# Kernel tuning notes

Hardware: AMD Instinct MI355X
Metric: run time of the kernel (lower is better)

The kernel has to match this reference:

```python
import jax, jax.numpy as jnp
import numpy as np

N_NODES = 50000
N_EDGES = 800000
IN_DIM = 64
HID = 256
EDGE_DIM = 6
NEG_SLOPE = 0.2


def setup_inputs() -> dict:
    key = jax.random.key(0)
    ks = jax.random.split(key, 16)
    glorot = lambda k, shp: jax.random.normal(k, shp, jnp.float32) * jnp.sqrt(2.0 / (shp[0] + shp[-1]))
    x = jax.random.normal(ks[0], (N_NODES, IN_DIM), jnp.float32)
    edge_index = jax.random.randint(ks[1], (2, N_EDGES), 0, N_NODES, dtype=jnp.int32)
    edge_attr = jax.random.normal(ks[2], (N_EDGES, EDGE_DIM), jnp.float32)
    return {
        "x": x,
        "edge_index": edge_index,
        "edge_attr": edge_attr,
        # layer 1 (heads=1)
        "W1": glorot(ks[3], (IN_DIM, HID)),
        "att_src1": glorot(ks[4], (HID,)),
        "att_dst1": glorot(ks[5], (HID,)),
        "We1": glorot(ks[6], (EDGE_DIM, HID)),
        "att_e1": glorot(ks[7], (HID,)),
        "b1": jnp.zeros((HID,), jnp.float32),
        # layer 2
        "W2": glorot(ks[8], (HID, HID)),
        "att_src2": glorot(ks[9], (HID,)),
        "att_dst2": glorot(ks[10], (HID,)),
        "We2": glorot(ks[11], (EDGE_DIM, HID)),
        "att_e2": glorot(ks[12], (HID,)),
        "b2": jnp.zeros((HID,), jnp.float32),
    }


def gat_conv(x, src, dst, edge_attr, W, att_src, att_dst, We, att_e, b):
    # PyG GATConv, heads=1, add_self_loops=False, edge features in attention only
    h = x @ W                              # [N, C]
    a_src = h @ att_src                    # [N]
    a_dst = h @ att_dst                    # [N]
    a_edge = (edge_attr @ We) @ att_e      # [E]
    alpha = a_src[src] + a_dst[dst] + a_edge            # [E]
    alpha = jax.nn.leaky_relu(alpha, NEG_SLOPE)
    # softmax over edges sharing the same destination node
    amax = jax.ops.segment_max(alpha, dst, num_segments=N_NODES)
    amax = jnp.where(jnp.isneginf(amax), 0.0, amax)
    ex = jnp.exp(alpha - amax[dst])
    denom = jax.ops.segment_sum(ex, dst, num_segments=N_NODES)
    alpha = ex / (denom[dst] + 1e-16)
    msg = h[src] * alpha[:, None]          # [E, C]
    out = jax.ops.segment_sum(msg, dst, num_segments=N_NODES)  # [N, C]
    return out + b


def reference(x, edge_index, edge_attr, W1, att_src1, att_dst1, We1, att_e1, b1,
              W2, att_src2, att_dst2, We2, att_e2, b2):
    src, dst = edge_index[0], edge_index[1]
    h = jax.nn.relu(gat_conv(x, src, dst, edge_attr, W1, att_src1, att_dst1, We1, att_e1, b1))
    # dropout(p=0.2) is identity in eval mode
    out = gat_conv(h, src, dst, edge_attr, W2, att_src2, att_dst2, We2, att_e2, b2)
    return out  # out_proj is Identity (out_dim=None)
```

## Files before the change

### kernel.cpp

```cpp
#include <hip/hip_runtime.h>
#include <hip/hip_bf16.h>

#define N_NODES_C 50000
#define N_EDGES_C 800000
#define IN_DIM_C 64
#define HID_C 256
#define EDGE_DIM_C 6
#define NEG_SLOPE_C 0.2f

typedef short short8 __attribute__((ext_vector_type(8)));
typedef float f32x4 __attribute__((ext_vector_type(4)));

static __device__ __forceinline__ float b2f(unsigned short u) {
    union { unsigned int i; float f; } x;
    x.i = ((unsigned int)u) << 16;
    return x.f;
}
static __device__ __forceinline__ unsigned short f2b(float f) {
    union { __hip_bfloat16 h; unsigned short u; } x;
    x.h = __float2bfloat16(f);
    return x.u;
}

__global__ void k_prep(const float* __restrict__ W1, const float* __restrict__ W2,
                       unsigned short* __restrict__ W1t, unsigned short* __restrict__ W2t,
                       const float* __restrict__ We1, const float* __restrict__ atte1,
                       const float* __restrict__ We2, const float* __restrict__ atte2,
                       float* __restrict__ v) {
    int tid = threadIdx.x;
    int i = blockIdx.x * blockDim.x + tid;
    if (i < IN_DIM_C * HID_C) {
        int k = i >> 8, n = i & 255;
        W1t[n * IN_DIM_C + k] = f2b(W1[i]);
    }
    if (i < HID_C * HID_C) {
        int k = i >> 8, n = i & 255;
        W2t[n * HID_C + k] = f2b(W2[i]);
    }
    if (blockIdx.x == 255) {
        __shared__ float red[256];
        for (int layer = 0; layer < 2; ++layer) {
            const float* We = layer ? We2 : We1;
            const float* ae = layer ? atte2 : atte1;
            for (int k = 0; k < EDGE_DIM_C; ++k) {
                red[tid] = We[k * HID_C + tid] * ae[tid];
                __syncthreads();
                for (int s = 128; s > 0; s >>= 1) {
                    if (tid < s) red[tid] += red[tid + s];
                    __syncthreads();
                }
                if (tid == 0) v[layer * 8 + k] = red[0];
                __syncthreads();
            }
        }
    }
}

__global__ void k_pre(const int* __restrict__ dst, const float* __restrict__ eattr,
                      const float* __restrict__ v, int* __restrict__ deg,
                      float* __restrict__ ae1, float* __restrict__ ae2) {
    int e = blockIdx.x * blockDim.x + threadIdx.x;
    if (e >= N_EDGES_C) return;
    atomicAdd(&deg[dst[e]], 1);
    float a1 = 0.f, a2 = 0.f;
#pragma unroll
    for (int k = 0; k < EDGE_DIM_C; ++k) {
        float ea = eattr[e * EDGE_DIM_C + k];
        a1 += ea * v[k];
        a2 += ea * v[8 + k];
    }
    ae1[e] = a1;
    ae2[e] = a2;
}

__global__ void k_scan1(const int* __restrict__ deg, int* __restrict__ offs,
                        int* __restrict__ bsum) {
    __shared__ int tmp[256];
    int b = blockIdx.x, tid = threadIdx.x;
    int i = b * 256 + tid;
    int v = (i < N_NODES_C) ? deg[i] : 0;
    tmp[tid] = v;
    __syncthreads();
    for (int d = 1; d < 256; d <<= 1) {
        int t = (tid >= d) ? tmp[tid - d] : 0;
        __syncthreads();
        tmp[tid] += t;
        __syncthreads();
    }
    if (i < N_NODES_C) offs[i] = tmp[tid] - v;
    if (tid == 255) bsum[b] = tmp[255];
}
__global__ void k_scan2(const int* __restrict__ bsum, int* __restrict__ boff, int nb) {
    __shared__ int tmp[256];
    int tid = threadIdx.x;
    int v = (tid < nb) ? bsum[tid] : 0;
    tmp[tid] = v;
    __syncthreads();
    for (int d = 1; d < 256; d <<= 1) {
        int t = (tid >= d) ? tmp[tid - d] : 0;
        __syncthreads();
        tmp[tid] += t;
        __syncthreads();
    }
    if (tid < nb) boff[tid] = tmp[tid] - v;
}
__global__ void k_scan3(int* __restrict__ offs, const int* __restrict__ boff,
                        int* __restrict__ cur) {
    int b = blockIdx.x, tid = threadIdx.x;
    int i = b * 256 + tid;
    if (i < N_NODES_C) {
        int o = offs[i] + boff[b];
        offs[i] = o;
        cur[i] = o;
    }
    if (i == 0) offs[N_NODES_C] = N_EDGES_C;
}

__global__ void k_perm(const int* __restrict__ dst, int* __restrict__ cur,
                       int* __restrict__ perm) {
    int e = blockIdx.x * blockDim.x + threadIdx.x;
    if (e >= N_EDGES_C) return;
    int pos = atomicAdd(&cur[dst[e]], 1);
    perm[pos] = e;
}

__global__ void k_gather(const int* __restrict__ perm, const int* __restrict__ src,
                         const float* __restrict__ ae1, const float* __restrict__ ae2,
                         int* __restrict__ ssrc, float* __restrict__ sae1,
                         float* __restrict__ sae2) {
    int p = blockIdx.x * blockDim.x + threadIdx.x;
    if (p >= N_EDGES_C) return;
    int e = perm[p];
    ssrc[p] = src[e];
    sae1[p] = ae1[e];
    sae2[p] = ae2[e];
}

template <int KT, bool SRCF32>
__global__ __launch_bounds__(256) void k_gemm_mfma(const void* __restrict__ Xv,
                                                   const unsigned short* __restrict__ Wt,
                                                   unsigned short* __restrict__ H,
                                                   const float* __restrict__ att_s,
                                                   const float* __restrict__ att_d,
                                                   float* __restrict__ asrc,
                                                   float* __restrict__ adst) {
    __shared__ unsigned short As[64 * 64];
    __shared__ unsigned short Bs[256 * 64];
    __shared__ float ds[4][64];
    __shared__ float dd[4][64];
    int tid = threadIdx.x;
    int w = tid >> 6, l = tid & 63;
    int lr = l & 15, lg = l >> 4;
    long mbase = (long)blockIdx.x * 64;

    float asv[4], adv[4];
#pragma unroll
    for (int ni = 0; ni < 4; ++ni) {
        int col = w * 64 + ni * 16 + lr;
        asv[ni] = att_s[col];
        adv[ni] = att_d[col];
    }

    f32x4 acc[4][4];
#pragma unroll
    for (int mi = 0; mi < 4; ++mi)
#pragma unroll
        for (int ni = 0; ni < 4; ++ni) acc[mi][ni] = (f32x4){0.f, 0.f, 0.f, 0.f};

    for (int k0 = 0; k0 < KT; k0 += 64) {
#pragma unroll
        for (int p = 0; p < 2; ++p) {
            int r = p * 32 + (tid >> 3);
            int c8 = tid & 7;
            long row = mbase + r;
            short8 val = {0, 0, 0, 0, 0, 0, 0, 0};
            if (row < N_NODES_C) {
                if (SRCF32) {
                    const float* Xf = (const float*)Xv;
                    const f32x4* p4 = (const f32x4*)&Xf[row * KT + k0 + c8 * 8];
                    f32x4 a0 = p4[0], a1 = p4[1];
#pragma unroll
                    for (int q = 0; q < 4; ++q) val[q] = (short)f2b(a0[q]);
#pragma unroll
                    for (int q = 0; q < 4; ++q) val[4 + q] = (short)f2b(a1[q]);
                } else {
                    const unsigned short* Xb = (const unsigned short*)Xv;
                    val = *(const short8*)&Xb[row * KT + k0 + c8 * 8];
                }
            }
            *(short8*)&As[r * 64 + ((c8 ^ (r & 7)) * 8)] = val;
        }
        {
            int n = tid;
#pragma unroll
            for (int c8 = 0; c8 < 8; ++c8) {
                *(short8*)&Bs[n * 64 + ((c8 ^ (n & 7)) * 8)] =
                    *(const short8*)&Wt[(long)n * KT + k0 + c8 * 8];
            }
        }
        __syncthreads();
#pragma unroll
        for (int kk = 0; kk < 2; ++kk) {
            int cblk = kk * 4 + lg;
            short8 a[4], b[4];
#pragma unroll
            for (int mi = 0; mi < 4; ++mi) {
                int R = mi * 16 + lr;
                a[mi] = *(const short8*)&As[R * 64 + ((cblk ^ (R & 7)) * 8)];
            }
#pragma unroll
            for (int ni = 0; ni < 4; ++ni) {
                int Nr = w * 64 + ni * 16 + lr;
                b[ni] = *(const short8*)&Bs[Nr * 64 + ((cblk ^ (Nr & 7)) * 8)];
            }
#pragma unroll
            for (int mi = 0; mi < 4; ++mi)
#pragma unroll
                for (int ni = 0; ni < 4; ++ni)
                    acc[mi][ni] = __builtin_amdgcn_mfma_f32_16x16x32_bf16(a[mi], b[ni],
                                                                          acc[mi][ni], 0, 0, 0);
        }
        __syncthreads();
    }

#pragma unroll
    for (int mi = 0; mi < 4; ++mi) {
#pragma unroll
        for (int r = 0; r < 4; ++r) {
            int rowl = mi * 16 + lg * 4 + r;
            long row = mbase + rowl;
            float ps = 0.f, pd = 0.f;
#pragma unroll
            for (int ni = 0; ni < 4; ++ni) {
                float h = acc[mi][ni][r];
                ps += h * asv[ni];
                pd += h * adv[ni];
            }
#pragma unroll
            for (int o = 1; o < 16; o <<= 1) {
                ps += __shfl_xor(ps, o, 16);
                pd += __shfl_xor(pd, o, 16);
            }
            if (lr == 0) {
                ds[w][rowl] = ps;
                dd[w][rowl] = pd;
            }
            if (row < N_NODES_C) {
#pragma unroll
                for (int ni = 0; ni < 4; ++ni) {
                    H[row * HID_C + w * 64 + ni * 16 + lr] = f2b(acc[mi][ni][r]);
                }
            }
        }
    }
    __syncthreads();
    if (tid < 64) {
        long row = mbase + tid;
        if (row < N_NODES_C) {
            asrc[row] = ds[0][tid] + ds[1][tid] + ds[2][tid] + ds[3][tid];
            adst[row] = dd[0][tid] + dd[1][tid] + dd[2][tid] + dd[3][tid];
        }
    }
}

__global__ __launch_bounds__(256) void k_aggr2(const int* __restrict__ offs,
                                               const int* __restrict__ ssrc,
                                               const float* __restrict__ sae,
                                               const float* __restrict__ asrc,
                                               const float* __restrict__ adst,
                                               const unsigned short* __restrict__ H,
                                               const float* __restrict__ bias,
                                               void* __restrict__ outp, int mode) {
    int tid = threadIdx.x;
    int hw = tid >> 5;
    int l = tid & 31;
    int node = blockIdx.x * 8 + hw;
    int off0 = offs[node];
    int deg = offs[node + 1] - off0;
    float adi = adst[node];

    int sidx0 = 0, sidx1 = 0;
    float w0 = 0.f, w1 = 0.f;
    if (l < deg) {
        sidx0 = ssrc[off0 + l];
        float a = asrc[sidx0] + adi + sae[off0 + l];
        a = (a > 0.f) ? a : NEG_SLOPE_C * a;
        w0 = __expf(a);
    }
    if (32 + l < deg) {
        sidx1 = ssrc[off0 + 32 + l];
        float a = asrc[sidx1] + adi + sae[off0 + 32 + l];
        a = (a > 0.f) ? a : NEG_SLOPE_C * a;
        w1 = __expf(a);
    }
    float s = w0 + w1;
    for (int j = 64 + l; j < deg; j += 32) {
        int si = ssrc[off0 + j];
        float a = asrc[si] + adi + sae[off0 + j];
        a = (a > 0.f) ? a : NEG_SLOPE_C * a;
        s += __expf(a);
    }
#pragma unroll
    for (int o = 16; o > 0; o >>= 1) s += __shfl_xor(s, o, 32);
    float inv = 1.0f / (s + 1e-16f);

    int c8 = l * 8;
    float acc[8];
#pragma unroll
    for (int q = 0; q < 8; ++q) acc[q] = 0.f;

    auto fetch = [&](int j, int& si, float& wv) {
        if (j < 32) {
            si = __shfl(sidx0, j, 32);
            wv = __shfl(w0, j, 32);
        } else if (j < 64) {
            si = __shfl(sidx1, j - 32, 32);
            wv = __shfl(w1, j - 32, 32);
        } else {
            si = ssrc[off0 + j];
            float a = asrc[si] + adi + sae[off0 + j];
            a = (a > 0.f) ? a : NEG_SLOPE_C * a;
            wv = __expf(a);
        }
    };

    int j = 0;
    for (; j + 7 < deg; j += 8) {
        int ii[8];
        float uu[8];
#pragma unroll
        for (int q = 0; q < 8; ++q) fetch(j + q, ii[q], uu[q]);
        short8 h[8];
#pragma unroll
        for (int q = 0; q < 8; ++q) h[q] = *(const short8*)&H[(long)ii[q] * HID_C + c8];
#pragma unroll
        for (int t = 0; t < 8; ++t)
#pragma unroll
            for (int q = 0; q < 8; ++q) acc[q] += uu[t] * b2f((unsigned short)h[t][q]);
    }
    for (; j + 3 < deg; j += 4) {
        int ii[4];
        float uu[4];
#pragma unroll
        for (int q = 0; q < 4; ++q) fetch(j + q, ii[q], uu[q]);
        short8 h[4];
#pragma unroll
        for (int q = 0; q < 4; ++q) h[q] = *(const short8*)&H[(long)ii[q] * HID_C + c8];
#pragma unroll
        for (int t = 0; t < 4; ++t)
#pragma unroll
            for (int q = 0; q < 8; ++q) acc[q] += uu[t] * b2f((unsigned short)h[t][q]);
    }
    for (; j < deg; ++j) {
        int i0;
        float u0;
        fetch(j, i0, u0);
        short8 h0 = *(const short8*)&H[(long)i0 * HID_C + c8];
#pragma unroll
        for (int q = 0; q < 8; ++q) acc[q] += u0 * b2f((unsigned short)h0[q]);
    }

    const f32x4* b4 = (const f32x4*)&bias[c8];
    f32x4 bv0 = b4[0], bv1 = b4[1];
    if (mode == 1) {
        unsigned short* o16 = (unsigned short*)outp;
        short8 r;
#pragma unroll
        for (int q = 0; q < 4; ++q)
            r[q] = (short)f2b(fmaxf(acc[q] * inv + bv0[q], 0.f));
#pragma unroll
        for (int q = 0; q < 4; ++q)
            r[4 + q] = (short)f2b(fmaxf(acc[4 + q] * inv + bv1[q], 0.f));
        *(short8*)&o16[(long)node * HID_C + c8] = r;
    } else {
        float* o32 = (float*)outp;
        f32x4 r0, r1;
#pragma unroll
        for (int q = 0; q < 4; ++q) r0[q] = acc[q] * inv + bv0[q];
#pragma unroll
        for (int q = 0; q < 4; ++q) r1[q] = acc[4 + q] * inv + bv1[q];
        *(f32x4*)&o32[(long)node * HID_C + c8] = r0;
        *(f32x4*)&o32[(long)node * HID_C + c8 + 4] = r1;
    }
}

extern "C" void kernel_launch(void* const* d_in, const int* in_sizes, int n_in,
                              void* d_out, int out_size, void* d_ws, size_t ws_size,
                              hipStream_t stream) {
    const float* x     = (const float*)d_in[0];
    const int*   ei    = (const int*)d_in[1];
    const float* eattr = (const float*)d_in[2];
    const float* W1    = (const float*)d_in[3];
    const float* atts1 = (const float*)d_in[4];
    const float* attd1 = (const float*)d_in[5];
    const float* We1   = (const float*)d_in[6];
    const float* atte1 = (const float*)d_in[7];
    const float* b1    = (const float*)d_in[8];
    const float* W2    = (const float*)d_in[9];
    const float* atts2 = (const float*)d_in[10];
    const float* attd2 = (const float*)d_in[11];
    const float* We2   = (const float*)d_in[12];
    const float* atte2 = (const float*)d_in[13];
    const float* b2    = (const float*)d_in[14];
    float* out = (float*)d_out;

    char* ws = (char*)d_ws;
    size_t off = 0;
    auto alloc = [&](size_t bytes) -> void* {
        void* p = ws + off;
        off = (off + bytes + 255) & ~(size_t)255;
        return p;
    };
    int*   deg  = (int*)alloc((size_t)N_NODES_C * 4);
    int*   offs = (int*)alloc(((size_t)N_NODES_C + 1) * 4);
    int*   cur  = (int*)alloc((size_t)N_NODES_C * 4);
    int*   perm = (int*)alloc((size_t)N_EDGES_C * 4);
    int*   ssrc = (int*)alloc((size_t)N_EDGES_C * 4);
    float* ae1  = (float*)alloc((size_t)N_EDGES_C * 4);
    float* ae2  = (float*)alloc((size_t)N_EDGES_C * 4);
    float* sae1 = (float*)alloc((size_t)N_EDGES_C * 4);
    float* sae2 = (float*)alloc((size_t)N_EDGES_C * 4);
    float* asrc = (float*)alloc((size_t)N_NODES_C * 4);
    float* adst = (float*)alloc((size_t)N_NODES_C * 4);
    float* v    = (float*)alloc(64);
    int*   bsum = (int*)alloc(256 * 4);
    int*   boff = (int*)alloc(257 * 4);
    unsigned short* W1t = (unsigned short*)alloc((size_t)HID_C * IN_DIM_C * 2);
    unsigned short* W2t = (unsigned short*)alloc((size_t)HID_C * HID_C * 2);
    unsigned short* h1  = (unsigned short*)alloc((size_t)N_NODES_C * HID_C * 2);
    unsigned short* g1  = (unsigned short*)alloc((size_t)N_NODES_C * HID_C * 2);

    const int* src = ei;
    const int* dst = ei + N_EDGES_C;
    int nb = (N_NODES_C + 255) / 256;

    hipMemsetAsync(deg, 0, (size_t)N_NODES_C * 4, stream);

    k_prep<<<256, 256, 0, stream>>>(W1, W2, W1t, W2t, We1, atte1, We2, atte2, v);
    k_pre<<<(N_EDGES_C + 255) / 256, 256, 0, stream>>>(dst, eattr, v, deg, ae1, ae2);
    k_scan1<<<nb, 256, 0, stream>>>(deg, offs, bsum);
    k_scan2<<<1, 256, 0, stream>>>(bsum, boff, nb);
    k_scan3<<<nb, 256, 0, stream>>>(offs, boff, cur);
    k_perm<<<(N_EDGES_C + 255) / 256, 256, 0, stream>>>(dst, cur, perm);
    k_gather<<<(N_EDGES_C + 255) / 256, 256, 0, stream>>>(perm, src, ae1, ae2,
                                                          ssrc, sae1, sae2);

    int gemm_grid = (N_NODES_C + 63) / 64;
    k_gemm_mfma<IN_DIM_C, true><<<gemm_grid, 256, 0, stream>>>(x, W1t, h1, atts1, attd1,
                                                               asrc, adst);
    k_aggr2<<<N_NODES_C / 8, 256, 0, stream>>>(offs, ssrc, sae1, asrc, adst, h1, b1, g1, 1);
    k_gemm_mfma<HID_C, false><<<gemm_grid, 256, 0, stream>>>(g1, W2t, h1, atts2, attd2,
                                                             asrc, adst);
    k_aggr2<<<N_NODES_C / 8, 256, 0, stream>>>(offs, ssrc, sae2, asrc, adst, h1, b2, out, 0);
}
```

Before: 306.1 us.

## Split aggregation into normalization pass and column-sliced gather with packed edge records

```diff
diff --git a/kernel.cpp b/kernel.cpp
--- a/kernel.cpp
+++ b/kernel.cpp
@@ -263,124 +263,91 @@
     }
 }
 
-__global__ __launch_bounds__(256) void k_aggr2(const int* __restrict__ offs,
-                                               const int* __restrict__ ssrc,
-                                               const float* __restrict__ sae,
-                                               const float* __restrict__ asrc,
-                                               const float* __restrict__ adst,
-                                               const unsigned short* __restrict__ H,
-                                               const float* __restrict__ bias,
-                                               void* __restrict__ outp, int mode) {
+__global__ __launch_bounds__(256) void k_norm(const int* __restrict__ offs,
+                                              const int* __restrict__ ssrc,
+                                              const float* __restrict__ sae,
+                                              const float* __restrict__ asrc,
+                                              const float* __restrict__ adst,
+                                              float* __restrict__ wts,
+                                              unsigned int* __restrict__ enc) {
     int tid = threadIdx.x;
-    int hw = tid >> 5;
-    int l = tid & 31;
+    int hw = tid >> 5, l = tid & 31;
     int node = blockIdx.x * 8 + hw;
     int off0 = offs[node];
     int deg = offs[node + 1] - off0;
     float adi = adst[node];
-
-    int sidx0 = 0, sidx1 = 0;
-    float w0 = 0.f, w1 = 0.f;
-    if (l < deg) {
-        sidx0 = ssrc[off0 + l];
-        float a = asrc[sidx0] + adi + sae[off0 + l];
-        a = (a > 0.f) ? a : NEG_SLOPE_C * a;
-        w0 = __expf(a);
-    }
-    if (32 + l < deg) {
-        sidx1 = ssrc[off0 + 32 + l];
-        float a = asrc[sidx1] + adi + sae[off0 + 32 + l];
-        a = (a > 0.f) ? a : NEG_SLOPE_C * a;
-        w1 = __expf(a);
-    }
-    float s = w0 + w1;
-    for (int j = 64 + l; j < deg; j += 32) {
+    float s = 0.f;
+    for (int j = l; j < deg; j += 32) {
         int si = ssrc[off0 + j];
         float a = asrc[si] + adi + sae[off0 + j];
         a = (a > 0.f) ? a : NEG_SLOPE_C * a;
-        s += __expf(a);
+        float w = __expf(a);
+        wts[off0 + j] = w;
+        s += w;
     }
 #pragma unroll
     for (int o = 16; o > 0; o >>= 1) s += __shfl_xor(s, o, 32);
     float inv = 1.0f / (s + 1e-16f);
-
-    int c8 = l * 8;
-    float acc[8];
-#pragma unroll
-    for (int q = 0; q < 8; ++q) acc[q] = 0.f;
-
-    auto fetch = [&](int j, int& si, float& wv) {
-        if (j < 32) {
-            si = __shfl(sidx0, j, 32);
-            wv = __shfl(w0, j, 32);
-        } else if (j < 64) {
-            si = __shfl(sidx1, j - 32, 32);
-            wv = __shfl(w1, j - 32, 32);
-        } else {
-            si = ssrc[off0 + j];
-            float a = asrc[si] + adi + sae[off0 + j];
-            a = (a > 0.f) ? a : NEG_SLOPE_C * a;
-            wv = __expf(a);
-        }
-    };
-
+    for (int j = l; j < deg; j += 32) {
+        unsigned int sv = ((unsigned int)ssrc[off0 + j]) << 16;
+        enc[off0 + j] = sv | (unsigned int)f2b(wts[off0 + j] * inv);
+    }
+}
+
+__global__ __launch_bounds__(256) void k_aggrslice(const int* __restrict__ offs,
+                                                   const unsigned int* __restrict__ enc,
+                                                   const unsigned short* __restrict__ H,
+                                                   const float* __restrict__ bias,
+                                                   void* __restrict__ outp, int mode) {
+    int tid = threadIdx.x;
+    int slice = blockIdx.x & 7;
+    int grp = blockIdx.x >> 3;
+    int g = tid >> 4;
+    int l = tid & 15;
+    int node = grp * 16 + g;
+    int off0 = offs[node];
+    int deg = offs[node + 1] - off0;
+    int ce = slice * 32 + l * 2;
+    const unsigned int* ep = enc + off0;
+
+    float a0 = 0.f, a1 = 0.f;
     int j = 0;
-    for (; j + 7 < deg; j += 8) {
-        int ii[8];
-        float uu[8];
-#pragma unroll
-        for (int q = 0; q < 8; ++q) fetch(j + q, ii[q], uu[q]);
-        short8 h[8];
-#pragma unroll
-        for (int q = 0; q < 8; ++q) h[q] = *(const short8*)&H[(long)ii[q] * HID_C + c8];
-#pragma unroll
-        for (int t = 0; t < 8; ++t)
-#pragma unroll
-            for (int q = 0; q < 8; ++q) acc[q] += uu[t] * b2f((unsigned short)h[t][q]);
-    }
     for (; j + 3 < deg; j += 4) {
-        int ii[4];
-        float uu[4];
-#pragma unroll
-        for (int q = 0; q < 4; ++q) fetch(j + q, ii[q], uu[q]);
-        short8 h[4];
-#pragma unroll
-        for (int q = 0; q < 4; ++q) h[q] = *(const short8*)&H[(long)ii[q] * HID_C + c8];
-#pragma unroll
-        for (int t = 0; t < 4; ++t)
-#pragma unroll
-            for (int q = 0; q < 8; ++q) acc[q] += uu[t] * b2f((unsigned short)h[t][q]);
+        unsigned int e0 = __builtin_nontemporal_load(ep + j);
+        unsigned int e1 = __builtin_nontemporal_load(ep + j + 1);
+        unsigned int e2 = __builtin_nontemporal_load(ep + j + 2);
+        unsigned int e3 = __builtin_nontemporal_load(ep + j + 3);
+        ushort2 h0 = *(const ushort2*)&H[(e0 >> 16) * HID_C + ce];
+        ushort2 h1 = *(const ushort2*)&H[(e1 >> 16) * HID_C + ce];
+        ushort2 h2 = *(const ushort2*)&H[(e2 >> 16) * HID_C + ce];
+        ushort2 h3 = *(const ushort2*)&H[(e3 >> 16) * HID_C + ce];
+        float w0 = b2f((unsigned short)(e0 & 0xffffu));
+        float w1 = b2f((unsigned short)(e1 & 0xffffu));
+        float w2 = b2f((unsigned short)(e2 & 0xffffu));
+        float w3 = b2f((unsigned short)(e3 & 0xffffu));
+        a0 += w0 * b2f(h0.x) + w1 * b2f(h1.x) + w2 * b2f(h2.x) + w3 * b2f(h3.x);
+        a1 += w0 * b2f(h0.y) + w1 * b2f(h1.y) + w2 * b2f(h2.y) + w3 * b2f(h3.y);
     }
     for (; j < deg; ++j) {
-        int i0;
-        float u0;
-        fetch(j, i0, u0);
-        short8 h0 = *(const short8*)&H[(long)i0 * HID_C + c8];
-#pragma unroll
-        for (int q = 0; q < 8; ++q) acc[q] += u0 * b2f((unsigned short)h0[q]);
-    }
-
-    const f32x4* b4 = (const f32x4*)&bias[c8];
-    f32x4 bv0 = b4[0], bv1 = b4[1];
+        unsigned int e0 = __builtin_nontemporal_load(ep + j);
+        ushort2 h0 = *(const ushort2*)&H[(e0 >> 16) * HID_C + ce];
+        float w0 = b2f((unsigned short)(e0 & 0xffffu));
+        a0 += w0 * b2f(h0.x);
+        a1 += w0 * b2f(h0.y);
+    }
+
+    float r0 = a0 + bias[ce];
+    float r1 = a1 + bias[ce + 1];
     if (mode == 1) {
-        unsigned short* o16 = (unsigned short*)outp;
-        short8 r;
-#pragma unroll
-        for (int q = 0; q < 4; ++q)
-            r[q] = (short)f2b(fmaxf(acc[q] * inv + bv0[q], 0.f));
-#pragma unroll
-        for (int q = 0; q < 4; ++q)
-            r[4 + q] = (short)f2b(fmaxf(acc[4 + q] * inv + bv1[q], 0.f));
-        *(short8*)&o16[(long)node * HID_C + c8] = r;
+        ushort2 r;
+        r.x = f2b(fmaxf(r0, 0.f));
+        r.y = f2b(fmaxf(r1, 0.f));
+        *(ushort2*)&((unsigned short*)outp)[(long)node * HID_C + ce] = r;
     } else {
-        float* o32 = (float*)outp;
-        f32x4 r0, r1;
-#pragma unroll
-        for (int q = 0; q < 4; ++q) r0[q] = acc[q] * inv + bv0[q];
-#pragma unroll
-        for (int q = 0; q < 4; ++q) r1[q] = acc[4 + q] * inv + bv1[q];
-        *(f32x4*)&o32[(long)node * HID_C + c8] = r0;
-        *(f32x4*)&o32[(long)node * HID_C + c8 + 4] = r1;
+        float2 r;
+        r.x = r0;
+        r.y = r1;
+        *(float2*)&((float*)outp)[(long)node * HID_C + ce] = r;
     }
 }
 
@@ -430,6 +397,9 @@
     unsigned short* h1  = (unsigned short*)alloc((size_t)N_NODES_C * HID_C * 2);
     unsigned short* g1  = (unsigned short*)alloc((size_t)N_NODES_C * HID_C * 2);
 
+    float*        wts = ae1;
+    unsigned int* enc = (unsigned int*)ae2;
+
     const int* src = ei;
     const int* dst = ei + N_EDGES_C;
     int nb = (N_NODES_C + 255) / 256;
@@ -446,10 +416,13 @@
                                                           ssrc, sae1, sae2);
 
     int gemm_grid = (N_NODES_C + 63) / 64;
+    int aggr_grid = (N_NODES_C / 16) * 8;
     k_gemm_mfma<IN_DIM_C, true><<<gemm_grid, 256, 0, stream>>>(x, W1t, h1, atts1, attd1,
                                                                asrc, adst);
-    k_aggr2<<<N_NODES_C / 8, 256, 0, stream>>>(offs, ssrc, sae1, asrc, adst, h1, b1, g1, 1);
+    k_norm<<<N_NODES_C / 8, 256, 0, stream>>>(offs, ssrc, sae1, asrc, adst, wts, enc);
+    k_aggrslice<<<aggr_grid, 256, 0, stream>>>(offs, enc, h1, b1, g1, 1);
     k_gemm_mfma<HID_C, false><<<gemm_grid, 256, 0, stream>>>(g1, W2t, h1, atts2, attd2,
                                                              asrc, adst);
-    k_aggr2<<<N_NODES_C / 8, 256, 0, stream>>>(offs, ssrc, sae2, asrc, adst, h1, b2, out, 0);
-}
+    k_norm<<<N_NODES_C / 8, 256, 0, stream>>>(offs, ssrc, sae2, asrc, adst, wts, enc);
+    k_aggrslice<<<aggr_grid, 256, 0, stream>>>(offs, enc, h1, b2, out, 0);
+}
```

Result: slower. 504.5 us (+64.8%).

## Fuse layer-1 aggregation into layer-2 GEMM and merge edge prep with GEMM1

Applied to the files above, without the earlier changes.

```diff
diff --git a/kernel.cpp b/kernel.cpp
--- a/kernel.cpp
+++ b/kernel.cpp
@@ -22,13 +22,102 @@
     return x.u;
 }
 
+static __device__ __forceinline__ float aggr_node(int off0, int deg, float adi,
+                                                  const int* __restrict__ ssrc,
+                                                  const float* __restrict__ sae,
+                                                  const float* __restrict__ asrc,
+                                                  const unsigned short* __restrict__ H,
+                                                  int l, float* acc) {
+    int sidx0 = 0, sidx1 = 0;
+    float w0 = 0.f, w1 = 0.f;
+    if (l < deg) {
+        sidx0 = ssrc[off0 + l];
+        float a = asrc[sidx0] + adi + sae[off0 + l];
+        a = (a > 0.f) ? a : NEG_SLOPE_C * a;
+        w0 = __expf(a);
+    }
+    if (32 + l < deg) {
+        sidx1 = ssrc[off0 + 32 + l];
+        float a = asrc[sidx1] + adi + sae[off0 + 32 + l];
+        a = (a > 0.f) ? a : NEG_SLOPE_C * a;
+        w1 = __expf(a);
+    }
+    float s = w0 + w1;
+    for (int j = 64 + l; j < deg; j += 32) {
+        int si = ssrc[off0 + j];
+        float a = asrc[si] + adi + sae[off0 + j];
+        a = (a > 0.f) ? a : NEG_SLOPE_C * a;
+        s += __expf(a);
+    }
+#pragma unroll
+    for (int o = 16; o > 0; o >>= 1) s += __shfl_xor(s, o, 32);
+    float inv = 1.0f / (s + 1e-16f);
+
+    int c8 = l * 8;
+#pragma unroll
+    for (int q = 0; q < 8; ++q) acc[q] = 0.f;
+
+    auto fetch = [&](int j, int& si, float& wv) {
+        if (j < 32) {
+            si = __shfl(sidx0, j, 32);
+            wv = __shfl(w0, j, 32);
+        } else if (j < 64) {
+            si = __shfl(sidx1, j - 32, 32);
+            wv = __shfl(w1, j - 32, 32);
+        } else {
+            si = ssrc[off0 + j];
+            float a = asrc[si] + adi + sae[off0 + j];
+            a = (a > 0.f) ? a : NEG_SLOPE_C * a;
+            wv = __expf(a);
+        }
+    };
+
+    int j = 0;
+    for (; j + 7 < deg; j += 8) {
+        int ii[8];
+        float uu[8];
+#pragma unroll
+        for (int q = 0; q < 8; ++q) fetch(j + q, ii[q], uu[q]);
+        short8 h[8];
+#pragma unroll
+        for (int q = 0; q < 8; ++q) h[q] = *(const short8*)&H[(long)ii[q] * HID_C + c8];
+#pragma unroll
+        for (int t = 0; t < 8; ++t)
+#pragma unroll
+            for (int q = 0; q < 8; ++q) acc[q] += uu[t] * b2f((unsigned short)h[t][q]);
+    }
+    for (; j + 3 < deg; j += 4) {
+        int ii[4];
+        float uu[4];
+#pragma unroll
+        for (int q = 0; q < 4; ++q) fetch(j + q, ii[q], uu[q]);
+        short8 h[4];
+#pragma unroll
+        for (int q = 0; q < 4; ++q) h[q] = *(const short8*)&H[(long)ii[q] * HID_C + c8];
+#pragma unroll
+        for (int t = 0; t < 4; ++t)
+#pragma unroll
+            for (int q = 0; q < 8; ++q) acc[q] += uu[t] * b2f((unsigned short)h[t][q]);
+    }
+    for (; j < deg; ++j) {
+        int i0;
+        float u0;
+        fetch(j, i0, u0);
+        short8 h0 = *(const short8*)&H[(long)i0 * HID_C + c8];
+#pragma unroll
+        for (int q = 0; q < 8; ++q) acc[q] += u0 * b2f((unsigned short)h0[q]);
+    }
+    return inv;
+}
+
 __global__ void k_prep(const float* __restrict__ W1, const float* __restrict__ W2,
                        unsigned short* __restrict__ W1t, unsigned short* __restrict__ W2t,
                        const float* __restrict__ We1, const float* __restrict__ atte1,
                        const float* __restrict__ We2, const float* __restrict__ atte2,
-                       float* __restrict__ v) {
+                       float* __restrict__ v, int* __restrict__ deg) {
     int tid = threadIdx.x;
     int i = blockIdx.x * blockDim.x + tid;
+    if (i < N_NODES_C) deg[i] = 0;
     if (i < IN_DIM_C * HID_C) {
         int k = i >> 8, n = i & 255;
         W1t[n * IN_DIM_C + k] = f2b(W1[i]);
@@ -56,21 +145,143 @@
     }
 }
 
-__global__ void k_pre(const int* __restrict__ dst, const float* __restrict__ eattr,
-                      const float* __restrict__ v, int* __restrict__ deg,
-                      float* __restrict__ ae1, float* __restrict__ ae2) {
-    int e = blockIdx.x * blockDim.x + threadIdx.x;
-    if (e >= N_EDGES_C) return;
-    atomicAdd(&deg[dst[e]], 1);
-    float a1 = 0.f, a2 = 0.f;
-#pragma unroll
-    for (int k = 0; k < EDGE_DIM_C; ++k) {
-        float ea = eattr[e * EDGE_DIM_C + k];
-        a1 += ea * v[k];
-        a2 += ea * v[8 + k];
-    }
-    ae1[e] = a1;
-    ae2[e] = a2;
+#define GEMM1_BLOCKS 782
+
+__global__ __launch_bounds__(256) void k_pre_gemm1(
+    const float* __restrict__ X, const unsigned short* __restrict__ Wt,
+    unsigned short* __restrict__ H, const float* __restrict__ att_s,
+    const float* __restrict__ att_d, float* __restrict__ asrc,
+    float* __restrict__ adst,
+    const int* __restrict__ dst, const float* __restrict__ eattr,
+    const float* __restrict__ v, int* __restrict__ deg,
+    float* __restrict__ ae1, float* __restrict__ ae2) {
+    __shared__ unsigned short As[64 * 64];
+    __shared__ unsigned short Bs[256 * 64];
+    __shared__ float ds[4][64];
+    __shared__ float dd[4][64];
+    int tid = threadIdx.x;
+
+    if (blockIdx.x >= GEMM1_BLOCKS) {
+        int e = (blockIdx.x - GEMM1_BLOCKS) * 256 + tid;
+        if (e < N_EDGES_C) {
+            atomicAdd(&deg[dst[e]], 1);
+            float a1 = 0.f, a2 = 0.f;
+#pragma unroll
+            for (int k = 0; k < EDGE_DIM_C; ++k) {
+                float ea = eattr[e * EDGE_DIM_C + k];
+                a1 += ea * v[k];
+                a2 += ea * v[8 + k];
+            }
+            ae1[e] = a1;
+            ae2[e] = a2;
+        }
+        return;
+    }
+
+    int w = tid >> 6, l = tid & 63;
+    int lr = l & 15, lg = l >> 4;
+    long mbase = (long)blockIdx.x * 64;
+
+    float asv[4], adv[4];
+#pragma unroll
+    for (int ni = 0; ni < 4; ++ni) {
+        int col = w * 64 + ni * 16 + lr;
+        asv[ni] = att_s[col];
+        adv[ni] = att_d[col];
+    }
+
+    f32x4 acc[4][4];
+#pragma unroll
+    for (int mi = 0; mi < 4; ++mi)
+#pragma unroll
+        for (int ni = 0; ni < 4; ++ni) acc[mi][ni] = (f32x4){0.f, 0.f, 0.f, 0.f};
+
+    {
+#pragma unroll
+        for (int p = 0; p < 2; ++p) {
+            int r = p * 32 + (tid >> 3);
+            int c8 = tid & 7;
+            long row = mbase + r;
+            short8 val = {0, 0, 0, 0, 0, 0, 0, 0};
+            if (row < N_NODES_C) {
+                const f32x4* p4 = (const f32x4*)&X[row * IN_DIM_C + c8 * 8];
+                f32x4 a0 = p4[0], a1 = p4[1];
+#pragma unroll
+                for (int q = 0; q < 4; ++q) val[q] = (short)f2b(a0[q]);
+#pragma unroll
+                for (int q = 0; q < 4; ++q) val[4 + q] = (short)f2b(a1[q]);
+            }
+            *(short8*)&As[r * 64 + ((c8 ^ (r & 7)) * 8)] = val;
+        }
+        int n = tid;
+#pragma unroll
+        for (int c8 = 0; c8 < 8; ++c8) {
+            *(short8*)&Bs[n * 64 + ((c8 ^ (n & 7)) * 8)] =
+                *(const short8*)&Wt[(long)n * IN_DIM_C + c8 * 8];
+        }
+        __syncthreads();
+#pragma unroll
+        for (int kk = 0; kk < 2; ++kk) {
+            int cblk = kk * 4 + lg;
+            short8 a[4], b[4];
+#pragma unroll
+            for (int mi = 0; mi < 4; ++mi) {
+                int R = mi * 16 + lr;
+                a[mi] = *(const short8*)&As[R * 64 + ((cblk ^ (R & 7)) * 8)];
+            }
+#pragma unroll
+            for (int ni = 0; ni < 4; ++ni) {
+                int Nr = w * 64 + ni * 16 + lr;
+                b[ni] = *(const short8*)&Bs[Nr * 64 + ((cblk ^ (Nr & 7)) * 8)];
+            }
+#pragma unroll
+            for (int mi = 0; mi < 4; ++mi)
+#pragma unroll
+                for (int ni = 0; ni < 4; ++ni)
+                    acc[mi][ni] = __builtin_amdgcn_mfma_f32_16x16x32_bf16(a[mi], b[ni],
+                                                                          acc[mi][ni], 0, 0, 0);
+        }
+        __syncthreads();
+    }
+
+#pragma unroll
+    for (int mi = 0; mi < 4; ++mi) {
+#pragma unroll
+        for (int r = 0; r < 4; ++r) {
+            int rowl = mi * 16 + lg * 4 + r;
+            long row = mbase + rowl;
+            float ps = 0.f, pd = 0.f;
+#pragma unroll
+            for (int ni = 0; ni < 4; ++ni) {
+                float h = acc[mi][ni][r];
+                ps += h * asv[ni];
+                pd += h * adv[ni];
+            }
+#pragma unroll
+            for (int o = 1; o < 16; o <<= 1) {
+                ps += __shfl_xor(ps, o, 16);
+                pd += __shfl_xor(pd, o, 16);
+            }
+            if (lr == 0) {
+                ds[w][rowl] = ps;
+                dd[w][rowl] = pd;
+            }
+            if (row < N_NODES_C) {
+#pragma unroll
+                for (int ni = 0; ni < 4; ++ni) {
+                    H[row * HID_C + w * 64 + ni * 16 + lr] = f2b(acc[mi][ni][r]);
+                }
+            }
+        }
+    }
+    __syncthreads();
+    if (tid < 64) {
+        long row = mbase + tid;
+        if (row < N_NODES_C) {
+            asrc[row] = ds[0][tid] + ds[1][tid] + ds[2][tid] + ds[3][tid];
+            adst[row] = dd[0][tid] + dd[1][tid] + dd[2][tid] + dd[3][tid];
+        }
+    }
 }
 
 __global__ void k_scan1(const int* __restrict__ deg, int* __restrict__ offs,
@@ -136,22 +347,48 @@
     sae2[p] = ae2[e];
 }
 
-template <int KT, bool SRCF32>
-__global__ __launch_bounds__(256) void k_gemm_mfma(const void* __restrict__ Xv,
-                                                   const unsigned short* __restrict__ Wt,
-                                                   unsigned short* __restrict__ H,
-                                                   const float* __restrict__ att_s,
-                                                   const float* __restrict__ att_d,
-                                                   float* __restrict__ asrc,
-                                                   float* __restrict__ adst) {
-    __shared__ unsigned short As[64 * 64];
+__global__ __launch_bounds__(256) void k_aggr_gemm(
+    const int* __restrict__ offs, const int* __restrict__ ssrc,
+    const float* __restrict__ sae, const float* __restrict__ asrc,
+    const float* __restrict__ adst, const unsigned short* __restrict__ H,
+    const float* __restrict__ bias, const unsigned short* __restrict__ Wt,
+    unsigned short* __restrict__ H2, const float* __restrict__ att_s,
+    const float* __restrict__ att_d, float* __restrict__ asrc2,
+    float* __restrict__ adst2) {
+    __shared__ unsigned short As[64 * 256];
     __shared__ unsigned short Bs[256 * 64];
     __shared__ float ds[4][64];
     __shared__ float dd[4][64];
     int tid = threadIdx.x;
-    int w = tid >> 6, l = tid & 63;
-    int lr = l & 15, lg = l >> 4;
     long mbase = (long)blockIdx.x * 64;
+
+    int hw = tid >> 5, l = tid & 31;
+    int c8 = l * 8;
+    for (int p = 0; p < 8; ++p) {
+        int rowl = p * 8 + hw;
+        long node = mbase + rowl;
+        short8 rowv = {0, 0, 0, 0, 0, 0, 0, 0};
+        if (node < N_NODES_C) {
+            int off0 = offs[node];
+            int deg = offs[node + 1] - off0;
+            float adi = adst[node];
+            float acc[8];
+            float inv = aggr_node(off0, deg, adi, ssrc, sae, asrc, H, l, acc);
+            const f32x4* b4 = (const f32x4*)&bias[c8];
+            f32x4 bv0 = b4[0], bv1 = b4[1];
+#pragma unroll
+            for (int q = 0; q < 4; ++q)
+                rowv[q] = (short)f2b(fmaxf(acc[q] * inv + bv0[q], 0.f));
+#pragma unroll
+            for (int q = 0; q < 4; ++q)
+                rowv[4 + q] = (short)f2b(fmaxf(acc[4 + q] * inv + bv1[q], 0.f));
+        }
+        *(short8*)&As[rowl * 256 + (l >> 3) * 64 + (((l & 7) ^ (rowl & 7)) * 8)] = rowv;
+    }
+    __syncthreads();
+
+    int w = tid >> 6, l64 = tid & 63;
+    int lr = l64 & 15, lg = l64 >> 4;
 
     float asv[4], adv[4];
 #pragma unroll
@@ -167,36 +404,12 @@
 #pragma unroll
         for (int ni = 0; ni < 4; ++ni) acc[mi][ni] = (f32x4){0.f, 0.f, 0.f, 0.f};
 
-    for (int k0 = 0; k0 < KT; k0 += 64) {
-#pragma unroll
-        for (int p = 0; p < 2; ++p) {
-            int r = p * 32 + (tid >> 3);
-            int c8 = tid & 7;
-            long row = mbase + r;
-            short8 val = {0, 0, 0, 0, 0, 0, 0, 0};
-            if (row < N_NODES_C) {
-                if (SRCF32) {
-                    const float* Xf = (const float*)Xv;
-                    const f32x4* p4 = (const f32x4*)&Xf[row * KT + k0 + c8 * 8];
-                    f32x4 a0 = p4[0], a1 = p4[1];
-#pragma unroll
-                    for (int q = 0; q < 4; ++q) val[q] = (short)f2b(a0[q]);
-#pragma unroll
-                    for (int q = 0; q < 4; ++q) val[4 + q] = (short)f2b(a1[q]);
-                } else {
-                    const unsigned short* Xb = (const unsigned short*)Xv;
-                    val = *(const short8*)&Xb[row * KT + k0 + c8 * 8];
-                }
-            }
-            *(short8*)&As[r * 64 + ((c8 ^ (r & 7)) * 8)] = val;
-        }
-        {
-            int n = tid;
-#pragma unroll
-            for (int c8 = 0; c8 < 8; ++c8) {
-                *(short8*)&Bs[n * 64 + ((c8 ^ (n & 7)) * 8)] =
-                    *(const short8*)&Wt[(long)n * KT + k0 + c8 * 8];
-            }
+    for (int k0 = 0; k0 < HID_C; k0 += 64) {
+        int n = tid;
+#pragma unroll
+        for (int cb = 0; cb < 8; ++cb) {
+            *(short8*)&Bs[n * 64 + ((cb ^ (n & 7)) * 8)] =
+                *(const short8*)&Wt[(long)n * HID_C + k0 + cb * 8];
         }
         __syncthreads();
 #pragma unroll
@@ -206,7 +419,7 @@
 #pragma unroll
             for (int mi = 0; mi < 4; ++mi) {
                 int R = mi * 16 + lr;
-                a[mi] = *(const short8*)&As[R * 64 + ((cblk ^ (R & 7)) * 8)];
+                a[mi] = *(const short8*)&As[R * 256 + k0 + ((cblk ^ (R & 7)) * 8)];
             }
 #pragma unroll
             for (int ni = 0; ni < 4; ++ni) {
@@ -248,7 +461,7 @@
             if (row < N_NODES_C) {
 #pragma unroll
                 for (int ni = 0; ni < 4; ++ni) {
-                    H[row * HID_C + w * 64 + ni * 16 + lr] = f2b(acc[mi][ni][r]);
+                    H2[row * HID_C + w * 64 + ni * 16 + lr] = f2b(acc[mi][ni][r]);
                 }
             }
         }
@@ -257,8 +470,8 @@
     if (tid < 64) {
         long row = mbase + tid;
         if (row < N_NODES_C) {
-            asrc[row] = ds[0][tid] + ds[1][tid] + ds[2][tid] + ds[3][tid];
-            adst[row] = dd[0][tid] + dd[1][tid] + dd[2][tid] + dd[3][tid];
+            asrc2[row] = ds[0][tid] + ds[1][tid] + ds[2][tid] + ds[3][tid];
+            adst2[row] = dd[0][tid] + dd[1][tid] + dd[2][tid] + dd[3][tid];
         }
     }
 }
@@ -270,7 +483,7 @@
                                                const float* __restrict__ adst,
                                                const unsigned short* __restrict__ H,
                                                const float* __restrict__ bias,
-                                               void* __restrict__ outp, int mode) {
+                                               float* __restrict__ out) {
     int tid = threadIdx.x;
     int hw = tid >> 5;
     int l = tid & 31;
@@ -278,110 +491,18 @@
     int off0 = offs[node];
     int deg = offs[node + 1] - off0;
     float adi = adst[node];
-
-    int sidx0 = 0, sidx1 = 0;
-    float w0 = 0.f, w1 = 0.f;
-    if (l < deg) {
-        sidx0 = ssrc[off0 + l];
-        float a = asrc[sidx0] + adi + sae[off0 + l];
-        a = (a > 0.f) ? a : NEG_SLOPE_C * a;
-        w0 = __expf(a);
-    }
-    if (32 + l < deg) {
-        sidx1 = ssrc[off0 + 32 + l];
-        float a = asrc[sidx1] + adi + sae[off0 + 32 + l];
-        a = (a > 0.f) ? a : NEG_SLOPE_C * a;
-        w1 = __expf(a);
-    }
-    float s = w0 + w1;
-    for (int j = 64 + l; j < deg; j += 32) {
-        int si = ssrc[off0 + j];
-        float a = asrc[si] + adi + sae[off0 + j];
-        a = (a > 0.f) ? a : NEG_SLOPE_C * a;
-        s += __expf(a);
-    }
-#pragma unroll
-    for (int o = 16; o > 0; o >>= 1) s += __shfl_xor(s, o, 32);
-    float inv = 1.0f / (s + 1e-16f);
-
+    float acc[8];
+    float inv = aggr_node(off0, deg, adi, ssrc, sae, asrc, H, l, acc);
     int c8 = l * 8;
-    float acc[8];
-#pragma unroll
-    for (int q = 0; q < 8; ++q) acc[q] = 0.f;
-
-    auto fetch = [&](int j, int& si, float& wv) {
-        if (j < 32) {
-            si = __shfl(sidx0, j, 32);
-            wv = __shfl(w0, j, 32);
-        } else if (j < 64) {
-            si = __shfl(sidx1, j - 32, 32);
-            wv = __shfl(w1, j - 32, 32);
-        } else {
-            si = ssrc[off0 + j];
-            float a = asrc[si] + adi + sae[off0 + j];
-            a = (a > 0.f) ? a : NEG_SLOPE_C * a;
-            wv = __expf(a);
-        }
-    };
-
-    int j = 0;
-    for (; j + 7 < deg; j += 8) {
-        int ii[8];
-        float uu[8];
-#pragma unroll
-        for (int q = 0; q < 8; ++q) fetch(j + q, ii[q], uu[q]);
-        short8 h[8];
-#pragma unroll
-        for (int q = 0; q < 8; ++q) h[q] = *(const short8*)&H[(long)ii[q] * HID_C + c8];
-#pragma unroll
-        for (int t = 0; t < 8; ++t)
-#pragma unroll
-            for (int q = 0; q < 8; ++q) acc[q] += uu[t] * b2f((unsigned short)h[t][q]);
-    }
-    for (; j + 3 < deg; j += 4) {
-        int ii[4];
-        float uu[4];
-#pragma unroll
-        for (int q = 0; q < 4; ++q) fetch(j + q, ii[q], uu[q]);
-        short8 h[4];
-#pragma unroll
-        for (int q = 0; q < 4; ++q) h[q] = *(const short8*)&H[(long)ii[q] * HID_C + c8];
-#pragma unroll
-        for (int t = 0; t < 4; ++t)
-#pragma unroll
-            for (int q = 0; q < 8; ++q) acc[q] += uu[t] * b2f((unsigned short)h[t][q]);
-    }
-    for (; j < deg; ++j) {
-        int i0;
-        float u0;
-        fetch(j, i0, u0);
-        short8 h0 = *(const short8*)&H[(long)i0 * HID_C + c8];
-#pragma unroll
-        for (int q = 0; q < 8; ++q) acc[q] += u0 * b2f((unsigned short)h0[q]);
-    }
-
     const f32x4* b4 = (const f32x4*)&bias[c8];
     f32x4 bv0 = b4[0], bv1 = b4[1];
-    if (mode == 1) {
-        unsigned short* o16 = (unsigned short*)outp;
-        short8 r;
-#pragma unroll
-        for (int q = 0; q < 4; ++q)
-            r[q] = (short)f2b(fmaxf(acc[q] * inv + bv0[q], 0.f));
-#pragma unroll
-        for (int q = 0; q < 4; ++q)
-            r[4 + q] = (short)f2b(fmaxf(acc[4 + q] * inv + bv1[q], 0.f));
-        *(short8*)&o16[(long)node * HID_C + c8] = r;
-    } else {
-        float* o32 = (float*)outp;
-        f32x4 r0, r1;
-#pragma unroll
-        for (int q = 0; q < 4; ++q) r0[q] = acc[q] * inv + bv0[q];
-#pragma unroll
-        for (int q = 0; q < 4; ++q) r1[q] = acc[4 + q] * inv + bv1[q];
-        *(f32x4*)&o32[(long)node * HID_C + c8] = r0;
-        *(f32x4*)&o32[(long)node * HID_C + c8 + 4] = r1;
-    }
+    f32x4 r0, r1;
+#pragma unroll
+    for (int q = 0; q < 4; ++q) r0[q] = acc[q] * inv + bv0[q];
+#pragma unroll
+    for (int q = 0; q < 4; ++q) r1[q] = acc[4 + q] * inv + bv1[q];
+    *(f32x4*)&out[(long)node * HID_C + c8] = r0;
+    *(f32x4*)&out[(long)node * HID_C + c8 + 4] = r1;
 }
 
 extern "C" void kernel_launch(void* const* d_in, const int* in_sizes, int n_in,
@@ -411,45 +532,43 @@
         off = (off + bytes + 255) & ~(size_t)255;
         return p;
     };
-    int*   deg  = (int*)alloc((size_t)N_NODES_C * 4);
-    int*   offs = (int*)alloc(((size_t)N_NODES_C + 1) * 4);
-    int*   cur  = (int*)alloc((size_t)N_NODES_C * 4);
-    int*   perm = (int*)alloc((size_t)N_EDGES_C * 4);
-    int*   ssrc = (int*)alloc((size_t)N_EDGES_C * 4);
-    float* ae1  = (float*)alloc((size_t)N_EDGES_C * 4);
-    float* ae2  = (float*)alloc((size_t)N_EDGES_C * 4);
-    float* sae1 = (float*)alloc((size_t)N_EDGES_C * 4);
-    float* sae2 = (float*)alloc((size_t)N_EDGES_C * 4);
-    float* asrc = (float*)alloc((size_t)N_NODES_C * 4);
-    float* adst = (float*)alloc((size_t)N_NODES_C * 4);
-    float* v    = (float*)alloc(64);
-    int*   bsum = (int*)alloc(256 * 4);
-    int*   boff = (int*)alloc(257 * 4);
+    int*   deg   = (int*)alloc((size_t)N_NODES_C * 4);
+    int*   offs  = (int*)alloc(((size_t)N_NODES_C + 1) * 4);
+    int*   cur   = (int*)alloc((size_t)N_NODES_C * 4);
+    int*   perm  = (int*)alloc((size_t)N_EDGES_C * 4);
+    int*   ssrc  = (int*)alloc((size_t)N_EDGES_C * 4);
+    float* ae1   = (float*)alloc((size_t)N_EDGES_C * 4);
+    float* ae2   = (float*)alloc((size_t)N_EDGES_C * 4);
+    float* sae1  = (float*)alloc((size_t)N_EDGES_C * 4);
+    float* sae2  = (float*)alloc((size_t)N_EDGES_C * 4);
+    float* asrc  = (float*)alloc((size_t)N_NODES_C * 4);
+    float* adst  = (float*)alloc((size_t)N_NODES_C * 4);
+    float* asrc2 = (float*)alloc((size_t)N_NODES_C * 4);
+    float* adst2 = (float*)alloc((size_t)N_NODES_C * 4);
+    float* v     = (float*)alloc(64);
+    int*   bsum  = (int*)alloc(256 * 4);
+    int*   boff  = (int*)alloc(257 * 4);
     unsigned short* W1t = (unsigned short*)alloc((size_t)HID_C * IN_DIM_C * 2);
     unsigned short* W2t = (unsigned short*)alloc((size_t)HID_C * HID_C * 2);
     unsigned short* h1  = (unsigned short*)alloc((size_t)N_NODES_C * HID_C * 2);
-    unsigned short* g1  = (unsigned short*)alloc((size_t)N_NODES_C * HID_C * 2);
+    unsigned short* h2  = (unsigned short*)alloc((size_t)N_NODES_C * HID_C * 2);
 
     const int* src = ei;
     const int* dst = ei + N_EDGES_C;
     int nb = (N_NODES_C + 255) / 256;
-
-    hipMemsetAsync(deg, 0, (size_t)N_NODES_C * 4, stream);
-
-    k_prep<<<256, 256, 0, stream>>>(W1, W2, W1t, W2t, We1, atte1, We2, atte2, v);
-    k_pre<<<(N_EDGES_C + 255) / 256, 256, 0, stream>>>(dst, eattr, v, deg, ae1, ae2);
+    int pre_blocks = (N_EDGES_C + 255) / 256;
+    int gemm_grid = (N_NODES_C + 63) / 64;
+
+    k_prep<<<256, 256, 0, stream>>>(W1, W2, W1t, W2t, We1, atte1, We2, atte2, v, deg);
+    k_pre_gemm1<<<GEMM1_BLOCKS + pre_blocks, 256, 0, stream>>>(
+        x, W1t, h1, atts1, attd1, asrc, adst, dst, eattr, v, deg, ae1, ae2);
     k_scan1<<<nb, 256, 0, stream>>>(deg, offs, bsum);
     k_scan2<<<1, 256, 0, stream>>>(bsum, boff, nb);
     k_scan3<<<nb, 256, 0, stream>>>(offs, boff, cur);
-    k_perm<<<(N_EDGES_C + 255) / 256, 256, 0, stream>>>(dst, cur, perm);
-    k_gather<<<(N_EDGES_C + 255) / 256, 256, 0, stream>>>(perm, src, ae1, ae2,
-                                                          ssrc, sae1, sae2);
-
-    int gemm_grid = (N_NODES_C + 63) / 64;
-    k_gemm_mfma<IN_DIM_C, true><<<gemm_grid, 256, 0, stream>>>(x, W1t, h1, atts1, attd1,
-                                                               asrc, adst);
-    k_aggr2<<<N_NODES_C / 8, 256, 0, stream>>>(offs, ssrc, sae1, asrc, adst, h1, b1, g1, 1);
-    k_gemm_mfma<HID_C, false><<<gemm_grid, 256, 0, stream>>>(g1, W2t, h1, atts2, attd2,
-                                                             asrc, adst);
-    k_aggr2<<<N_NODES_C / 8, 256, 0, stream>>>(offs, ssrc, sae2, asrc, adst, h1, b2, out, 0);
-}
+    k_perm<<<pre_blocks, 256, 0, stream>>>(dst, cur, perm);
+    k_gather<<<pre_blocks, 256, 0, stream>>>(perm, src, ae1, ae2, ssrc, sae1, sae2);
+
+    k_aggr_gemm<<<gemm_grid, 256, 0, stream>>>(offs, ssrc, sae1, asrc, adst, h1, b1,
+                                               W2t, h2, atts2, attd2, asrc2, adst2);
+    k_aggr2<<<N_NODES_C / 8, 256, 0, stream>>>(offs, ssrc, sae2, asrc2, adst2, h2, b2, out);
+}
```

After: 302.1 us. Within noise of the previous version (-1.3%).
